# Performance work log

Hardware: AMD Instinct MI355X
Metric: run time of the kernel (lower is better)

The kernel has to match this reference:

```python
import jax, jax.numpy as jnp
import numpy as np

B, S, D, H, RANK, NC = 2, 2048, 1024, 16, 128, 16
DH = D // H


def setup_inputs() -> dict:
    key = jax.random.key(0)
    ks = jax.random.split(key, 10)
    x = jax.random.normal(ks[0], (B, S, D), jnp.float32)
    # causal mask, broadcast over batch and heads like torch's [B,1,S,S]
    mask = jnp.tril(jnp.ones((S, S), dtype=bool))[None, None]
    # orthogonal-ish init approximated by scaled gaussian
    compress_neurons = jax.random.normal(ks[1], (NC, D, RANK), jnp.float32) / np.sqrt(D)
    router_Q = jax.random.normal(ks[2], (NC, D), jnp.float32) * 0.02
    router_K = jax.random.normal(ks[3], (NC, D), jnp.float32) * 0.02
    router_V = jax.random.normal(ks[4], (NC, D), jnp.float32) * 0.02
    wQ = jax.random.normal(ks[5], (D, RANK), jnp.float32) / np.sqrt(RANK)
    wK = jax.random.normal(ks[6], (D, RANK), jnp.float32) / np.sqrt(RANK)
    wV = jax.random.normal(ks[7], (D, RANK), jnp.float32) / np.sqrt(RANK)
    wO = jax.random.normal(ks[8], (D, D), jnp.float32) / np.sqrt(D)
    return {"x": x, "mask": mask, "compress_neurons": compress_neurons,
            "router_Q": router_Q, "router_K": router_K, "router_V": router_V,
            "wQ": wQ, "wK": wK, "wV": wV, "wO": wO}


def reference(x, mask, compress_neurons, router_Q, router_K, router_V, wQ, wK, wV, wO):
    def compress(router_w):
        # router scores -> softmax over all n_compress neurons
        w = jax.nn.softmax(jnp.einsum('bsd,nd->bsn', x, router_w), axis=-1)  # [B,S,NC]
        # softmax-weighted sum of all neuron projections (fused einsum)
        return jnp.einsum('bsd,ndr,bsn->bsr', x, compress_neurons, w)  # [B,S,RANK]

    hQ = compress(router_Q)
    hK = compress(router_K)
    hV = compress(router_V)
    # expand rank -> d_model (Linear weight [D,RANK]), then split heads
    Q = jnp.einsum('bsr,dr->bsd', hQ, wQ).reshape(B, S, H, DH).transpose(0, 2, 1, 3)
    K = jnp.einsum('bsr,dr->bsd', hK, wK).reshape(B, S, H, DH).transpose(0, 2, 1, 3)
    V = jnp.einsum('bsr,dr->bsd', hV, wV).reshape(B, S, H, DH).transpose(0, 2, 1, 3)
    scores = jnp.einsum('bhqd,bhkd->bhqk', Q, K) / np.sqrt(DH)  # [B,H,S,S]
    scores = jnp.where(mask, scores, -jnp.inf)
    attn = jax.nn.softmax(scores, axis=-1)
    attn_out = jnp.einsum('bhqk,bhkd->bhqd', attn, V)
    attn_out = attn_out.transpose(0, 2, 1, 3).reshape(B, S, D)
    # dropout omitted (eval mode / dropout=0)
    return jnp.einsum('bsd,ed->bse', attn_out, wO)
```

## Files before the change

kernel.cpp:

```cpp
#include <hip/hip_runtime.h>
#include <hip/hip_bf16.h>
#include <math.h>

#define B_ 2
#define S_ 2048
#define D_ 1024
#define H_ 16
#define RANK_ 128
#define NC_ 16
#define DH_ 64
#define T_ (B_*S_)
#define NZ_ 2176

typedef __attribute__((ext_vector_type(8))) __bf16 bf16x8;
typedef __attribute__((ext_vector_type(8))) unsigned short u16x8;
typedef __attribute__((ext_vector_type(4))) float f32x4;

#if __has_builtin(__builtin_amdgcn_exp2f)
#define EXP2F(x) __builtin_amdgcn_exp2f(x)
#else
#define EXP2F(x) exp2f(x)
#endif

__device__ __forceinline__ unsigned short f2bu(float f) {
    __hip_bfloat16 h = __float2bfloat16(f);
    unsigned short u; __builtin_memcpy(&u, &h, 2); return u;
}
__device__ __forceinline__ float bu2f(unsigned short u) {
    __hip_bfloat16 h; __builtin_memcpy(&h, &u, 2); return __bfloat162float(h);
}

__device__ __forceinline__ void gl_lds16(const unsigned short* g, unsigned short* l) {
    __builtin_amdgcn_global_load_lds(
        (const __attribute__((address_space(1))) void*)g,
        (__attribute__((address_space(3))) void*)l, 16, 0, 0);
}

__device__ __forceinline__ bool sniff_f32(const unsigned* __restrict__ p) {
    int votes = 0;
    #pragma unroll
    for (int i = 0; i < 64; i++) {
        unsigned e = (p[i] >> 23) & 0xFFu;
        votes += (e >= 0x60u && e <= 0x8Fu) ? 1 : 0;
    }
    return votes >= 32;
}

struct Cvt { const void* src[9]; unsigned short* dst[9]; const void* C; unsigned short* Ct; };

__global__ __launch_bounds__(256) void k_inputs(Cvt cv,
    const unsigned* __restrict__ probe)
{
    bool f32 = sniff_f32(probe);
    if (blockIdx.x < 512) {
        int bid = blockIdx.x;
        int d0 = (bid & 15) * 64, r0 = ((bid >> 4) & 1) * 64, n = bid >> 5;
        __shared__ unsigned short tile[64][65];
        for (int idx = threadIdx.x; idx < 4096; idx += 256) {
            int row = idx >> 6, col = idx & 63;
            size_t si = ((size_t)n*D_ + d0 + row)*RANK_ + r0 + col;
            tile[row][col] = f32 ? f2bu(((const float*)cv.C)[si])
                                 : ((const unsigned short*)cv.C)[si];
        }
        __syncthreads();
        for (int idx = threadIdx.x; idx < 4096; idx += 256) {
            int row = idx >> 6, col = idx & 63;
            cv.Ct[((size_t)(n*RANK_ + r0 + row))*D_ + d0 + col] = tile[col][row];
        }
        return;
    }
    const int offs[9] = {0, 4194304, 4210688, 4227072, 4243456,
                         4259840, 4390912, 4521984, 4653056};
    const int total = 5701632;
    int nconv = gridDim.x - 512;
    int stride = nconv * 256;
    for (int i = (blockIdx.x - 512) * 256 + threadIdx.x; i < total; i += stride) {
        int seg = 0;
        #pragma unroll
        for (int s = 1; s < 9; s++) seg += (i >= offs[s]) ? 1 : 0;
        int local = i - offs[seg];
        const void* sp = cv.src[seg];
        unsigned short v = 0;
        if (sp) v = f32 ? f2bu(((const float*)sp)[local]) : ((const unsigned short*)sp)[local];
        cv.dst[seg][local] = v;
    }
}

template<int MT, int MODE>
__global__ __launch_bounds__(256) void k_mfma_gemm(const unsigned short* __restrict__ A,
    const unsigned short* __restrict__ Bm, void* __restrict__ Cout,
    const unsigned* __restrict__ probe, int M, int N, int K)
{
    bool f32out = false;
    if (MODE == 2) f32out = sniff_f32(probe);
    __shared__ __align__(16) unsigned short As[MT*32*32];
    __shared__ __align__(16) unsigned short Bs[128*32];
    const int tid = threadIdx.x;
    const int wv = tid >> 6, lane = tid & 63;
    const int wm = (wv >> 1) * (MT*16), wn = (wv & 1) * 64;
    const int quad = lane >> 4, l16 = lane & 15;
    const int m0 = blockIdx.x * (MT*32), n0 = blockIdx.y * 128;

    const f32x4 z4 = {0.f, 0.f, 0.f, 0.f};
    f32x4 acc[MT][4];
    #pragma unroll
    for (int i = 0; i < MT; i++)
        #pragma unroll
        for (int j = 0; j < 4; j++) acc[i][j] = z4;

    for (int k0 = 0; k0 < K; k0 += 32) {
        __syncthreads();
        #pragma unroll
        for (int c = 0; c < MT/2; c++) {
            int idx = wv*64 + c*256 + lane;
            gl_lds16(A + (size_t)(m0 + (idx >> 2))*K + k0 + (idx & 3)*8,
                     &As[(wv*64 + c*256)*8]);
        }
        #pragma unroll
        for (int c = 0; c < 2; c++) {
            int idx = wv*64 + c*256 + lane;
            gl_lds16(Bm + (size_t)(n0 + (idx >> 2))*K + k0 + (idx & 3)*8,
                     &Bs[(wv*64 + c*256)*8]);
        }
        __syncthreads();
        bf16x8 af[MT], bfr[4];
        #pragma unroll
        for (int mt = 0; mt < MT; mt++) af[mt]  = *(const bf16x8*)&As[(wm + mt*16 + l16)*32 + quad*8];
        #pragma unroll
        for (int nt = 0; nt < 4; nt++) bfr[nt] = *(const bf16x8*)&Bs[(wn + nt*16 + l16)*32 + quad*8];
        #pragma unroll
        for (int mt = 0; mt < MT; mt++)
            #pragma unroll
            for (int nt = 0; nt < 4; nt++)
                acc[mt][nt] = __builtin_amdgcn_mfma_f32_16x16x32_bf16(af[mt], bfr[nt], acc[mt][nt], 0, 0, 0);
    }
    #pragma unroll
    for (int mt = 0; mt < MT; mt++)
        #pragma unroll
        for (int nt = 0; nt < 4; nt++) {
            int col = n0 + wn + nt*16 + l16;
            #pragma unroll
            for (int r = 0; r < 4; r++) {
                int rowg = m0 + wm + mt*16 + quad*4 + r;
                float v = acc[mt][nt][r];
                if (MODE == 2 && f32out) ((float*)Cout)[(size_t)rowg*N + col] = v;
                else  ((unsigned short*)Cout)[(size_t)rowg*N + col] = f2bu(v);
            }
        }
}

__global__ __launch_bounds__(256) void k_qkv2(const unsigned short* __restrict__ h3,
    const unsigned short* __restrict__ wqkv, unsigned short* __restrict__ QKb,
    unsigned short* __restrict__ Vtg)
{
    __shared__ __align__(16) unsigned short As[128*32];
    __shared__ __align__(16) unsigned short Bs[128*32];
    const int tid = threadIdx.x;
    const int wv = tid >> 6, lane = tid & 63;
    const int wm = (wv >> 1) * 64, wn = (wv & 1) * 64;
    const int quad = lane >> 4, l16 = lane & 15;

    const bool vt = (blockIdx.x >= 512);
    int m0, n0;
    const unsigned short *A, *Bm;
    float scale = 1.f;
    if (!vt) {
        int id = blockIdx.x;
        m0 = (id & 31) * 128;
        n0 = (id >> 5) * 128;
        int w = n0 >> 10;
        A  = h3 + (size_t)w * T_ * RANK_ + (size_t)m0 * RANK_;
        Bm = wqkv + (size_t)w * D_ * RANK_ + (size_t)(n0 & 1023) * RANK_;
        if (w == 0) scale = 0.125f * 1.44269504f;
    } else {
        int id = blockIdx.x - 512;
        m0 = (id & 7) * 128;
        n0 = (id >> 3) * 128;
        A  = wqkv + (size_t)2 * D_ * RANK_ + (size_t)m0 * RANK_;
        Bm = h3 + (size_t)2 * T_ * RANK_ + (size_t)n0 * RANK_;
    }

    const f32x4 z4 = {0.f, 0.f, 0.f, 0.f};
    f32x4 acc[4][4];
    #pragma unroll
    for (int i = 0; i < 4; i++)
        #pragma unroll
        for (int j = 0; j < 4; j++) acc[i][j] = z4;

    for (int k0 = 0; k0 < RANK_; k0 += 32) {
        __syncthreads();
        #pragma unroll
        for (int c = 0; c < 2; c++) {
            int idx = wv*64 + c*256 + lane;
            gl_lds16(A  + (size_t)(idx >> 2)*RANK_ + k0 + (idx & 3)*8,
                     &As[(wv*64 + c*256)*8]);
            gl_lds16(Bm + (size_t)(idx >> 2)*RANK_ + k0 + (idx & 3)*8,
                     &Bs[(wv*64 + c*256)*8]);
        }
        __syncthreads();
        bf16x8 af[4], bfr[4];
        #pragma unroll
        for (int mt = 0; mt < 4; mt++) af[mt]  = *(const bf16x8*)&As[(wm + mt*16 + l16)*32 + quad*8];
        #pragma unroll
        for (int nt = 0; nt < 4; nt++) bfr[nt] = *(const bf16x8*)&Bs[(wn + nt*16 + l16)*32 + quad*8];
        #pragma unroll
        for (int mt = 0; mt < 4; mt++)
            #pragma unroll
            for (int nt = 0; nt < 4; nt++)
                acc[mt][nt] = __builtin_amdgcn_mfma_f32_16x16x32_bf16(af[mt], bfr[nt], acc[mt][nt], 0, 0, 0);
    }
    #pragma unroll
    for (int mt = 0; mt < 4; mt++)
        #pragma unroll
        for (int nt = 0; nt < 4; nt++) {
            #pragma unroll
            for (int r = 0; r < 4; r++) {
                int rowg = m0 + wm + mt*16 + quad*4 + r;
                int col  = n0 + wn + nt*16 + l16;
                float v = acc[mt][nt][r] * scale;
                if (!vt) {
                    QKb[(size_t)(col >> 10)*T_*D_ + (size_t)rowg*D_ + (col & 1023)]
                        = f2bu(v);
                } else {
                    size_t vrow = (size_t)((col >> 11)*H_ + (rowg >> 6))*64 + (rowg & 63);
                    Vtg[vrow*S_ + (col & 2047)] = f2bu(v);
                }
            }
        }
}

__global__ __launch_bounds__(256) void k_hreduce(const unsigned short* __restrict__ z,
    unsigned short* __restrict__ h)
{
    int t0 = blockIdx.x * 2;
    int tg = threadIdx.x >> 7, r = threadIdx.x & 127;
    int t = t0 + tg;
    __shared__ float sc[2][48];
    __shared__ float wl[2][3][16];
    if (threadIdx.x < 96) {
        int tk = threadIdx.x / 48, j = threadIdx.x % 48;
        sc[tk][j] = bu2f(z[(size_t)(t0 + tk)*NZ_ + 2048 + j]);
    }
    __syncthreads();
    if (threadIdx.x < 6) {
        int tk = threadIdx.x / 3, w = threadIdx.x % 3;
        float m = -INFINITY;
        for (int n = 0; n < 16; n++) m = fmaxf(m, sc[tk][w*16 + n]);
        float s = 0.f, e[16];
        for (int n = 0; n < 16; n++) { e[n] = __expf(sc[tk][w*16 + n] - m); s += e[n]; }
        float inv = 1.f / s;
        for (int n = 0; n < 16; n++) wl[tk][w][n] = e[n] * inv;
    }
    __syncthreads();
    const unsigned short* zr = z + (size_t)t * NZ_;
    float acc[3] = {0.f, 0.f, 0.f};
    #pragma unroll
    for (int n = 0; n < NC_; n++) {
        float zv = bu2f(zr[n*RANK_ + r]);
        #pragma unroll
        for (int w = 0; w < 3; w++) acc[w] += wl[tg][w][n] * zv;
    }
    #pragma unroll
    for (int w = 0; w < 3; w++) h[((size_t)w*T_ + t)*RANK_ + r] = f2bu(acc[w]);
}

__global__ __launch_bounds__(256) void k_flash_mfma(const unsigned short* __restrict__ Qm,
    const unsigned short* __restrict__ Km, const unsigned short* __restrict__ Vtg,
    unsigned short* __restrict__ Om)
{
    const int p = blockIdx.x, hh = blockIdx.y, b = blockIdx.z;
    __shared__ __align__(16) unsigned short Ks[2][128*64];
    __shared__ __align__(16) unsigned short Vs[2][64*128];
    __shared__ __align__(16) unsigned short Ps[64*128];
    const int tid = threadIdx.x;
    const int w = tid >> 6, lane = tid & 63;
    const int quad = lane >> 4, l16 = lane & 15;
    const size_t base  = ((size_t)b * S_) * D_ + (size_t)hh * DH_;
    const size_t vbase = (size_t)((b*H_ + hh) * 64) * S_;
    const f32x4 z4 = {0.f, 0.f, 0.f, 0.f};

    for (int rep = 0; rep < 2; rep++) {
        const int qt = rep ? (31 - p) : p;

        bf16x8 aq[2];
        #pragma unroll
        for (int s = 0; s < 2; s++)
            aq[s] = *(const bf16x8*)(Qm + base + (size_t)(qt*64 + w*16 + l16)*D_ + s*32 + quad*8);

        f32x4 oacc[4];
        #pragma unroll
        for (int nt = 0; nt < 4; nt++) oacc[nt] = z4;
        float lsum[4] = {0.f, 0.f, 0.f, 0.f};

        const int nkt = (qt >> 1) + 1;

        __syncthreads();
        #pragma unroll
        for (int c = 0; c < 4; c++) {
            int idx = c*256 + tid;
            int row = idx >> 3, j = (idx & 7) ^ (row & 7);
            gl_lds16(Km + base + (size_t)row*D_ + j*8, &Ks[0][(c*256 + (w<<6))*8]);
        }
        #pragma unroll
        for (int c = 0; c < 4; c++) {
            int idx = c*256 + tid;
            int row = idx >> 4, j = (idx & 15) ^ (row & 7);
            gl_lds16(Vtg + vbase + (size_t)row*S_ + j*8, &Vs[0][(c*256 + (w<<6))*8]);
        }

        for (int kt = 0; kt < nkt; kt++) {
            const int cur = kt & 1;
            __syncthreads();

            if (kt + 1 < nkt) {
                #pragma unroll
                for (int c = 0; c < 4; c++) {
                    int idx = c*256 + tid;
                    int row = idx >> 3, j = (idx & 7) ^ (row & 7);
                    gl_lds16(Km + base + (size_t)((kt+1)*128 + row)*D_ + j*8,
                             &Ks[1-cur][(c*256 + (w<<6))*8]);
                }
                #pragma unroll
                for (int c = 0; c < 4; c++) {
                    int idx = c*256 + tid;
                    int row = idx >> 4, j = (idx & 15) ^ (row & 7);
                    gl_lds16(Vtg + vbase + (size_t)row*S_ + (kt+1)*128 + j*8,
                             &Vs[1-cur][(c*256 + (w<<6))*8]);
                }
            }

            f32x4 sacc[8];
            #pragma unroll
            for (int nt = 0; nt < 8; nt++) sacc[nt] = z4;
            #pragma unroll
            for (int s = 0; s < 2; s++)
                #pragma unroll
                for (int nt = 0; nt < 8; nt++) {
                    int row = nt*16 + l16;
                    int cc = (s*4 + quad) ^ (row & 7);
                    bf16x8 bk = *(const bf16x8*)&Ks[cur][row*64 + cc*8];
                    sacc[nt] = __builtin_amdgcn_mfma_f32_16x16x32_bf16(aq[s], bk, sacc[nt], 0, 0, 0);
                }
            if (kt == (qt >> 1)) {
                #pragma unroll
                for (int nt = 0; nt < 8; nt++) {
                    int key = kt*128 + nt*16 + l16;
                    #pragma unroll
                    for (int r = 0; r < 4; r++)
                        if (key > qt*64 + w*16 + quad*4 + r) sacc[nt][r] = -INFINITY;
                }
            }
            #pragma unroll
            for (int r = 0; r < 4; r++) {
                float rs = 0.f;
                int tokl = quad*4 + r;
                #pragma unroll
                for (int nt = 0; nt < 8; nt++) {
                    float pv = EXP2F(sacc[nt][r]);
                    rs += pv;
                    int pc = (nt*2 + (l16 >> 3)) ^ (tokl & 7);
                    Ps[(w*16 + tokl)*128 + pc*8 + (l16 & 7)] = f2bu(pv);
                }
                lsum[r] += rs;
            }
            #pragma unroll
            for (int s = 0; s < 4; s++) {
                int pc = (s*4 + quad) ^ (l16 & 7);
                bf16x8 ap = *(const bf16x8*)&Ps[(w*16 + l16)*128 + pc*8];
                #pragma unroll
                for (int nt = 0; nt < 4; nt++) {
                    int row = nt*16 + l16;
                    int cc = (s*4 + quad) ^ (row & 7);
                    bf16x8 bv = *(const bf16x8*)&Vs[cur][row*128 + cc*8];
                    oacc[nt] = __builtin_amdgcn_mfma_f32_16x16x32_bf16(ap, bv, oacc[nt], 0, 0, 0);
                }
            }
        }
        #pragma unroll
        for (int r = 0; r < 4; r++) {
            float l = lsum[r];
            #pragma unroll
            for (int off = 1; off < 16; off <<= 1) l += __shfl_xor(l, off, 64);
            float inv = 1.f / l;
            int tok = qt*64 + w*16 + quad*4 + r;
            #pragma unroll
            for (int nt = 0; nt < 4; nt++)
                Om[base + (size_t)tok*D_ + nt*16 + l16] = f2bu(oacc[nt][r] * inv);
        }
    }
}

extern "C" void kernel_launch(void* const* d_in, const int* in_sizes, int n_in,
                              void* d_out, int out_size, void* d_ws, size_t ws_size,
                              hipStream_t stream)
{
    const unsigned* probe = (const unsigned*)d_in[0];

    unsigned short* u = (unsigned short*)d_ws;
    unsigned short* xc   = u;               size_t o = (size_t)T_*D_;
    unsigned short* wqkv = u + o;           o += (size_t)3*D_*RANK_;
    unsigned short* wOc  = u + o;           o += (size_t)D_*D_;
    unsigned short* Ct   = u + o;           o += (size_t)NZ_*D_;
    unsigned short* h3   = u + o;           o += (size_t)3*T_*RANK_;
    unsigned short* QKb  = u + o;           o += (size_t)2*T_*D_;
    unsigned short* Vtg  = u + o;           o += (size_t)T_*D_;
    unsigned short* z    = u + o;           o += (size_t)T_*NZ_;
    unsigned short* attnb= u + o;           o += (size_t)T_*D_;

    unsigned short* Rp = Ct + (size_t)2048*D_;
    unsigned short* Qb = QKb;
    unsigned short* Kb = QKb + (size_t)T_*D_;

    Cvt cv;
    cv.src[0] = d_in[0]; cv.dst[0] = xc;
    cv.src[1] = d_in[3]; cv.dst[1] = Rp;
    cv.src[2] = d_in[4]; cv.dst[2] = Rp + 16384;
    cv.src[3] = d_in[5]; cv.dst[3] = Rp + 32768;
    cv.src[4] = nullptr; cv.dst[4] = Rp + 49152;
    cv.src[5] = d_in[6]; cv.dst[5] = wqkv;
    cv.src[6] = d_in[7]; cv.dst[6] = wqkv + 131072;
    cv.src[7] = d_in[8]; cv.dst[7] = wqkv + 262144;
    cv.src[8] = d_in[9]; cv.dst[8] = wOc;
    cv.C = d_in[2]; cv.Ct = Ct;
    k_inputs<<<512 + 2048, 256, 0, stream>>>(cv, probe);

    k_mfma_gemm<4,0><<<dim3(T_/128, NZ_/128), 256, 0, stream>>>(
        xc, Ct, z, nullptr, T_, NZ_, D_);

    k_hreduce<<<T_/2, 256, 0, stream>>>(z, h3);

    k_qkv2<<<768, 256, 0, stream>>>(h3, wqkv, QKb, Vtg);

    k_flash_mfma<<<dim3(16, H_, B_), 256, 0, stream>>>(Qb, Kb, Vtg, attnb);

    k_mfma_gemm<2,2><<<dim3(T_/64, D_/128), 256, 0, stream>>>(
        attnb, wOc, d_out, probe, T_, D_, D_);
}
```

Measured before the change: 237.3 us.

## Rewrite flash attention with 32x32 MFMA and register-resident P via permlane swap

Restructures the attention kernel to use 32x32x16 MFMA tiles with 128-query blocks per workgroup and 64-key tiles. It computes S transposed so the exponentiated probabilities can be packed to bf16 and rearranged across lanes with permlane32 swaps, which removes the LDS round trip for P. The causal pairing of query tiles (two reps per block) is replaced by one tile per block in reverse order, and occupancy is hinted at two blocks per CU with a smaller LDS footprint. The risks are the new lane-layout logic and losing the load balance that the tile pairing provided.

```diff
diff --git a/kernel.cpp b/kernel.cpp
--- a/kernel.cpp
+++ b/kernel.cpp
@@ -15,6 +15,7 @@
 typedef __attribute__((ext_vector_type(8))) __bf16 bf16x8;
 typedef __attribute__((ext_vector_type(8))) unsigned short u16x8;
 typedef __attribute__((ext_vector_type(4))) float f32x4;
+typedef __attribute__((ext_vector_type(16))) float f32x16;
 
 #if __has_builtin(__builtin_amdgcn_exp2f)
 #define EXP2F(x) __builtin_amdgcn_exp2f(x)
@@ -34,6 +35,15 @@
     __builtin_amdgcn_global_load_lds(
         (const __attribute__((address_space(1))) void*)g,
         (__attribute__((address_space(3))) void*)l, 16, 0, 0);
+}
+
+__device__ __forceinline__ unsigned cvtpk_bf16(float lo, float hi) {
+    unsigned r;
+    asm("v_cvt_pk_bf16_f32 %0, %1, %2" : "=v"(r) : "v"(lo), "v"(hi));
+    return r;
+}
+__device__ __forceinline__ void plswap(unsigned &a, unsigned &b) {
+    asm("v_permlane32_swap_b32 %0, %1" : "+v"(a), "+v"(b));
 }
 
 __device__ __forceinline__ bool sniff_f32(const unsigned* __restrict__ p) {
@@ -264,129 +274,136 @@
     for (int w = 0; w < 3; w++) h[((size_t)w*T_ + t)*RANK_ + r] = f2bu(acc[w]);
 }
 
-__global__ __launch_bounds__(256) void k_flash_mfma(const unsigned short* __restrict__ Qm,
+__global__ __launch_bounds__(256, 2) void k_flash_mfma(const unsigned short* __restrict__ Qm,
     const unsigned short* __restrict__ Km, const unsigned short* __restrict__ Vtg,
     unsigned short* __restrict__ Om)
 {
-    const int p = blockIdx.x, hh = blockIdx.y, b = blockIdx.z;
-    __shared__ __align__(16) unsigned short Ks[2][128*64];
-    __shared__ __align__(16) unsigned short Vs[2][64*128];
-    __shared__ __align__(16) unsigned short Ps[64*128];
+    const int qt = 15 - blockIdx.x;
+    const int hh = blockIdx.y, b = blockIdx.z;
+    __shared__ __align__(16) unsigned short Ks[2][64*64];
+    __shared__ __align__(16) unsigned short Vs[2][64*64];
     const int tid = threadIdx.x;
     const int w = tid >> 6, lane = tid & 63;
-    const int quad = lane >> 4, l16 = lane & 15;
+    const int l32 = lane & 31, hi = lane >> 5;
     const size_t base  = ((size_t)b * S_) * D_ + (size_t)hh * DH_;
     const size_t vbase = (size_t)((b*H_ + hh) * 64) * S_;
-    const f32x4 z4 = {0.f, 0.f, 0.f, 0.f};
-
-    for (int rep = 0; rep < 2; rep++) {
-        const int qt = rep ? (31 - p) : p;
-
-        bf16x8 aq[2];
-        #pragma unroll
-        for (int s = 0; s < 2; s++)
-            aq[s] = *(const bf16x8*)(Qm + base + (size_t)(qt*64 + w*16 + l16)*D_ + s*32 + quad*8);
-
-        f32x4 oacc[4];
-        #pragma unroll
-        for (int nt = 0; nt < 4; nt++) oacc[nt] = z4;
-        float lsum[4] = {0.f, 0.f, 0.f, 0.f};
-
-        const int nkt = (qt >> 1) + 1;
-
-        __syncthreads();
-        #pragma unroll
-        for (int c = 0; c < 4; c++) {
-            int idx = c*256 + tid;
-            int row = idx >> 3, j = (idx & 7) ^ (row & 7);
-            gl_lds16(Km + base + (size_t)row*D_ + j*8, &Ks[0][(c*256 + (w<<6))*8]);
-        }
-        #pragma unroll
-        for (int c = 0; c < 4; c++) {
-            int idx = c*256 + tid;
-            int row = idx >> 4, j = (idx & 15) ^ (row & 7);
-            gl_lds16(Vtg + vbase + (size_t)row*S_ + j*8, &Vs[0][(c*256 + (w<<6))*8]);
-        }
-
-        for (int kt = 0; kt < nkt; kt++) {
-            const int cur = kt & 1;
-            __syncthreads();
-
-            if (kt + 1 < nkt) {
+    const int tokg = qt*128 + w*32 + l32;
+
+    bf16x8 aq[4];
+    #pragma unroll
+    for (int ks = 0; ks < 4; ks++)
+        aq[ks] = *(const bf16x8*)(Qm + base + (size_t)tokg*D_ + ks*16 + hi*8);
+
+    f32x16 oacc[2];
+    #pragma unroll
+    for (int db = 0; db < 2; db++)
+        #pragma unroll
+        for (int i = 0; i < 16; i++) oacc[db][i] = 0.f;
+    float lsum = 0.f;
+
+    const int nkt = 2*(qt + 1);
+
+    #pragma unroll
+    for (int c = 0; c < 2; c++) {
+        int idx = c*256 + tid;
+        int row = idx >> 3, j = (idx & 7) ^ (row & 7);
+        gl_lds16(Km + base + (size_t)row*D_ + j*8, &Ks[0][(c*256 + (w<<6))*8]);
+    }
+    #pragma unroll
+    for (int c = 0; c < 2; c++) {
+        int idx = c*256 + tid;
+        int row = idx >> 3, j = (idx & 7) ^ (row & 7);
+        gl_lds16(Vtg + vbase + (size_t)row*S_ + j*8, &Vs[0][(c*256 + (w<<6))*8]);
+    }
+
+    for (int kt = 0; kt < nkt; kt++) {
+        const int cur = kt & 1;
+        __syncthreads();
+
+        if (kt + 1 < nkt) {
+            #pragma unroll
+            for (int c = 0; c < 2; c++) {
+                int idx = c*256 + tid;
+                int row = idx >> 3, j = (idx & 7) ^ (row & 7);
+                gl_lds16(Km + base + (size_t)((kt+1)*64 + row)*D_ + j*8,
+                         &Ks[1-cur][(c*256 + (w<<6))*8]);
+            }
+            #pragma unroll
+            for (int c = 0; c < 2; c++) {
+                int idx = c*256 + tid;
+                int row = idx >> 3, j = (idx & 7) ^ (row & 7);
+                gl_lds16(Vtg + vbase + (size_t)row*S_ + (kt+1)*64 + j*8,
+                         &Vs[1-cur][(c*256 + (w<<6))*8]);
+            }
+        }
+
+        f32x16 sacc[2];
+        #pragma unroll
+        for (int kb = 0; kb < 2; kb++)
+            #pragma unroll
+            for (int i = 0; i < 16; i++) sacc[kb][i] = 0.f;
+        #pragma unroll
+        for (int ks = 0; ks < 4; ks++)
+            #pragma unroll
+            for (int kb = 0; kb < 2; kb++) {
+                int row = kb*32 + l32;
+                int c = (ks*2 + hi) ^ (row & 7);
+                bf16x8 ak = *(const bf16x8*)&Ks[cur][row*64 + c*8];
+                sacc[kb] = __builtin_amdgcn_mfma_f32_32x32x16_bf16(ak, aq[ks], sacc[kb], 0, 0, 0);
+            }
+
+        if (kt >= 2*qt) {
+            #pragma unroll
+            for (int kb = 0; kb < 2; kb++)
                 #pragma unroll
-                for (int c = 0; c < 4; c++) {
-                    int idx = c*256 + tid;
-                    int row = idx >> 3, j = (idx & 7) ^ (row & 7);
-                    gl_lds16(Km + base + (size_t)((kt+1)*128 + row)*D_ + j*8,
-                             &Ks[1-cur][(c*256 + (w<<6))*8]);
+                for (int r = 0; r < 16; r++) {
+                    int keyg = kt*64 + kb*32 + (r&3) + 8*(r>>2) + 4*hi;
+                    if (keyg > tokg) sacc[kb][r] = -INFINITY;
                 }
-                #pragma unroll
-                for (int c = 0; c < 4; c++) {
-                    int idx = c*256 + tid;
-                    int row = idx >> 4, j = (idx & 15) ^ (row & 7);
-                    gl_lds16(Vtg + vbase + (size_t)row*S_ + (kt+1)*128 + j*8,
-                             &Vs[1-cur][(c*256 + (w<<6))*8]);
-                }
-            }
-
-            f32x4 sacc[8];
-            #pragma unroll
-            for (int nt = 0; nt < 8; nt++) sacc[nt] = z4;
-            #pragma unroll
-            for (int s = 0; s < 2; s++)
-                #pragma unroll
-                for (int nt = 0; nt < 8; nt++) {
-                    int row = nt*16 + l16;
-                    int cc = (s*4 + quad) ^ (row & 7);
-                    bf16x8 bk = *(const bf16x8*)&Ks[cur][row*64 + cc*8];
-                    sacc[nt] = __builtin_amdgcn_mfma_f32_16x16x32_bf16(aq[s], bk, sacc[nt], 0, 0, 0);
-                }
-            if (kt == (qt >> 1)) {
-                #pragma unroll
-                for (int nt = 0; nt < 8; nt++) {
-                    int key = kt*128 + nt*16 + l16;
-                    #pragma unroll
-                    for (int r = 0; r < 4; r++)
-                        if (key > qt*64 + w*16 + quad*4 + r) sacc[nt][r] = -INFINITY;
-                }
-            }
-            #pragma unroll
-            for (int r = 0; r < 4; r++) {
-                float rs = 0.f;
-                int tokl = quad*4 + r;
-                #pragma unroll
-                for (int nt = 0; nt < 8; nt++) {
-                    float pv = EXP2F(sacc[nt][r]);
-                    rs += pv;
-                    int pc = (nt*2 + (l16 >> 3)) ^ (tokl & 7);
-                    Ps[(w*16 + tokl)*128 + pc*8 + (l16 & 7)] = f2bu(pv);
-                }
-                lsum[r] += rs;
-            }
-            #pragma unroll
-            for (int s = 0; s < 4; s++) {
-                int pc = (s*4 + quad) ^ (l16 & 7);
-                bf16x8 ap = *(const bf16x8*)&Ps[(w*16 + l16)*128 + pc*8];
-                #pragma unroll
-                for (int nt = 0; nt < 4; nt++) {
-                    int row = nt*16 + l16;
-                    int cc = (s*4 + quad) ^ (row & 7);
-                    bf16x8 bv = *(const bf16x8*)&Vs[cur][row*128 + cc*8];
-                    oacc[nt] = __builtin_amdgcn_mfma_f32_16x16x32_bf16(ap, bv, oacc[nt], 0, 0, 0);
-                }
-            }
-        }
-        #pragma unroll
-        for (int r = 0; r < 4; r++) {
-            float l = lsum[r];
-            #pragma unroll
-            for (int off = 1; off < 16; off <<= 1) l += __shfl_xor(l, off, 64);
-            float inv = 1.f / l;
-            int tok = qt*64 + w*16 + quad*4 + r;
-            #pragma unroll
-            for (int nt = 0; nt < 4; nt++)
-                Om[base + (size_t)tok*D_ + nt*16 + l16] = f2bu(oacc[nt][r] * inv);
-        }
+        }
+
+        bf16x8 pa[4];
+        #pragma unroll
+        for (int kb = 0; kb < 2; kb++) {
+            float pv[16];
+            #pragma unroll
+            for (int r = 0; r < 16; r++) {
+                pv[r] = EXP2F(sacc[kb][r]);
+                lsum += pv[r];
+            }
+            unsigned wd[8];
+            #pragma unroll
+            for (int j = 0; j < 8; j++) wd[j] = cvtpk_bf16(pv[2*j], pv[2*j+1]);
+            plswap(wd[0], wd[2]); plswap(wd[1], wd[3]);
+            plswap(wd[4], wd[6]); plswap(wd[5], wd[7]);
+            union { unsigned u[4]; bf16x8 v; } u0, u1;
+            u0.u[0]=wd[0]; u0.u[1]=wd[1]; u0.u[2]=wd[2]; u0.u[3]=wd[3];
+            u1.u[0]=wd[4]; u1.u[1]=wd[5]; u1.u[2]=wd[6]; u1.u[3]=wd[7];
+            pa[2*kb]   = u0.v;
+            pa[2*kb+1] = u1.v;
+        }
+
+        #pragma unroll
+        for (int ks = 0; ks < 4; ks++)
+            #pragma unroll
+            for (int db = 0; db < 2; db++) {
+                int row = db*32 + l32;
+                int c = (ks*2 + hi) ^ (row & 7);
+                bf16x8 bv = *(const bf16x8*)&Vs[cur][row*64 + c*8];
+                oacc[db] = __builtin_amdgcn_mfma_f32_32x32x16_bf16(pa[ks], bv, oacc[db], 0, 0, 0);
+            }
+    }
+
+    float l = lsum + __shfl_xor(lsum, 32);
+    float inv = 1.f / l;
+    #pragma unroll
+    for (int r = 0; r < 16; r++) {
+        int crow = (r&3) + 8*(r>>2) + 4*hi;
+        float invr = __shfl(inv, crow);
+        size_t rowo = base + (size_t)(qt*128 + w*32 + crow)*D_;
+        #pragma unroll
+        for (int db = 0; db < 2; db++)
+            Om[rowo + db*32 + l32] = f2bu(oacc[db][r] * invr);
     }
 }
 
```

After: 233.6 us. Within noise of the previous version (-1.6%).
